# Kernel tuning notes

Measured on AMD Instinct MI355X. Metric: run time of the kernel, lower is better.

Reference implementation:

```python
import jax, jax.numpy as jnp
import numpy as np

NUM_HOPS = 3
NUM_GRAPHS = 2048
N_NODES = 50000
N_EDGES = 2400000
HIDDEN = 128
EMB = 64
N_LAYERS = 3
N_MLP = 2
N_HEADS = 4


def setup_inputs() -> dict:
    key = jax.random.key(0)
    ks = iter(jax.random.split(key, 64))
    nk = lambda: next(ks)
    f = lambda shape: jax.random.normal(nk(), shape, dtype=jnp.float32) * 0.05
    inp = {}
    inp["atom_type"] = jax.random.randint(nk(), (N_NODES,), 0, 100)
    inp["hydrogen_count"] = jax.random.randint(nk(), (N_NODES,), 0, 9)
    inp["degree"] = jax.random.randint(nk(), (N_NODES,), 0, 8)
    inp["hybridization"] = jax.random.randint(nk(), (N_NODES,), 0, 8)
    inp["target"] = jax.random.randint(nk(), (N_EDGES,), 0, NUM_HOPS * N_NODES)
    inp["src"] = jax.random.randint(nk(), (N_EDGES,), 0, NUM_HOPS * N_NODES)
    inp["batch_indices"] = jnp.sort(jax.random.randint(nk(), (N_NODES,), 0, NUM_GRAPHS))
    # learned parameters
    inp["emb_atom"] = f((100, EMB))
    inp["emb_h"] = f((9, EMB))
    inp["emb_deg"] = f((8, EMB))
    inp["emb_hyb"] = f((8, EMB))
    inp["proj_w"] = f((4 * EMB, HIDDEN)); inp["proj_b"] = jnp.zeros((HIDDEN,), jnp.float32)
    IN = HIDDEN * (NUM_HOPS + 1)
    inp["shell_in_w"] = f((N_LAYERS, IN, HIDDEN)); inp["shell_in_b"] = jnp.zeros((N_LAYERS, HIDDEN), jnp.float32)
    inp["shell_mlp_w1"] = f((N_LAYERS, N_MLP, HIDDEN, HIDDEN)); inp["shell_mlp_b1"] = jnp.zeros((N_LAYERS, N_MLP, HIDDEN), jnp.float32)
    inp["shell_mlp_w2"] = f((N_LAYERS, N_MLP, HIDDEN, HIDDEN)); inp["shell_mlp_b2"] = jnp.zeros((N_LAYERS, N_MLP, HIDDEN), jnp.float32)
    inp["shell_skip_w"] = f((N_LAYERS, IN, HIDDEN)); inp["shell_skip_b"] = jnp.zeros((N_LAYERS, HIDDEN), jnp.float32)
    inp["attn_w"] = f((N_HEADS, HIDDEN)); inp["attn_b"] = jnp.zeros((N_HEADS,), jnp.float32)
    inp["temperature"] = jnp.array(1.0, jnp.float32)
    inp["ffn_w1"] = f((HIDDEN, HIDDEN)); inp["ffn_b1"] = jnp.zeros((HIDDEN,), jnp.float32)
    inp["ffn_w2"] = f((HIDDEN, HIDDEN)); inp["ffn_b2"] = jnp.zeros((HIDDEN,), jnp.float32)
    inp["ffn_w3"] = f((HIDDEN, 1)); inp["ffn_b3"] = jnp.zeros((1,), jnp.float32)
    return inp


def _forward(atom_type, hydrogen_count, degree, hybridization, target, src, batch_indices,
             emb_atom, emb_h, emb_deg, emb_hyb, proj_w, proj_b,
             shell_in_w, shell_in_b, shell_mlp_w1, shell_mlp_b1, shell_mlp_w2, shell_mlp_b2,
             shell_skip_w, shell_skip_b, attn_w, attn_b, temperature,
             ffn_w1, ffn_b1, ffn_w2, ffn_b2, ffn_w3, ffn_b3):
    act = jax.nn.silu
    n = atom_type.shape[0]
    # atom embedding: concat of 4 lookups -> projection (dropout off / eval mode)
    emb = jnp.concatenate([emb_atom[atom_type], emb_h[hydrogen_count],
                           emb_deg[degree], emb_hyb[hybridization]], axis=-1)  # [N, 4*EMB]
    x = act(emb @ proj_w + proj_b)  # [N, H]
    for l in range(N_LAYERS):
        # shell convolution: hop aggregation via gather + index_add over expanded [hops*N, H]
        expanded = jnp.tile(x, (NUM_HOPS, 1))                              # [hops*N, H]
        agg = jnp.zeros_like(expanded).at[target].add(expanded[src])
        hops = agg.reshape(NUM_HOPS, n, HIDDEN)                            # split into hop chunks
        feats = jnp.concatenate([x[None], hops], axis=0)                   # [hops+1, N, H]
        feats = jnp.moveaxis(feats, 0, 1).reshape(n, (NUM_HOPS + 1) * HIDDEN)  # cat([x, hop0..], -1)
        h = act(feats @ shell_in_w[l] + shell_in_b[l])
        gskip = feats @ shell_skip_w[l] + shell_skip_b[l]
        for m in range(N_MLP):
            skip = h
            h = act(h @ shell_mlp_w1[l, m] + shell_mlp_b1[l, m])
            h = h @ shell_mlp_w2[l, m] + shell_mlp_b2[l, m]
            h = h + skip
        x = h + gskip
    # multi-head attention pooling with scatter-softmax over graphs
    scores = (x @ attn_w.T + attn_b) / temperature                         # [N, heads]
    smax = jax.ops.segment_max(scores, batch_indices, num_segments=NUM_GRAPHS)
    ex = jnp.exp(scores - smax[batch_indices])
    denom = jax.ops.segment_sum(ex, batch_indices, num_segments=NUM_GRAPHS)
    w = ex / denom[batch_indices]                                          # [N, heads]
    weighted = (x[:, None, :] * w[:, :, None]).reshape(n, N_HEADS * HIDDEN)
    pooled = jax.ops.segment_sum(weighted, batch_indices, num_segments=NUM_GRAPHS)
    pooled = pooled.reshape(NUM_GRAPHS, N_HEADS, HIDDEN).mean(axis=1)      # mean over heads
    # FFN readout
    h = act(pooled @ ffn_w1 + ffn_b1)
    h = act(h @ ffn_w2 + ffn_b2)
    return h @ ffn_w3 + ffn_b3                                             # [G, 1]


def reference(atom_type, hydrogen_count, degree, hybridization, target, src, batch_indices,
              emb_atom, emb_h, emb_deg, emb_hyb, proj_w, proj_b,
              shell_in_w, shell_in_b, shell_mlp_w1, shell_mlp_b1, shell_mlp_w2, shell_mlp_b2,
              shell_skip_w, shell_skip_b, attn_w, attn_b, temperature,
              ffn_w1, ffn_b1, ffn_w2, ffn_b2, ffn_w3, ffn_b3):
    return _forward(atom_type, hydrogen_count, degree, hybridization, target, src, batch_indices,
                    emb_atom, emb_h, emb_deg, emb_hyb, proj_w, proj_b,
                    shell_in_w, shell_in_b, shell_mlp_w1, shell_mlp_b1, shell_mlp_w2, shell_mlp_b2,
                    shell_skip_w, shell_skip_b, attn_w, attn_b, temperature,
                    ffn_w1, ffn_b1, ffn_w2, ffn_b2, ffn_w3, ffn_b3)
```

## Files before the change

### kernel.cpp

```cpp
#include <hip/hip_runtime.h>
#include <math.h>

#define NN      50000
#define NNP     50048
#define NE      2400000
#define NHOPS   3
#define NG      2048
#define H       128
#define EMBD    64
#define NL      3
#define NMLP    2
#define NHEADS  4
#define NROWS   (NHOPS * NN)
#define BINSH   9
#define NBIN    293
#define CAPB    12288
#define ABLK    1024
#define DEPTH   32
#define STG     6144
#define LSTR    136
#define SENT    0xFFFFFFFFu

typedef __bf16 bf16x8 __attribute__((ext_vector_type(8)));
typedef __bf16 bf16x4 __attribute__((ext_vector_type(4)));
typedef float  f32x4  __attribute__((ext_vector_type(4)));

__device__ __forceinline__ float silu_f(float v) { return v / (1.0f + expf(-v)); }

__device__ __forceinline__ f32x4 mm(bf16x8 a, bf16x8 b, f32x4 c) {
    return __builtin_amdgcn_mfma_f32_16x16x32_bf16(a, b, c, 0, 0, 0);
}

__device__ __forceinline__ float blo(unsigned v) { return __builtin_bit_cast(float, v << 16); }
__device__ __forceinline__ float bhi(unsigned v) { return __builtin_bit_cast(float, v & 0xffff0000u); }
__device__ __forceinline__ unsigned pk2(float a, float b) {
    unsigned short ua = __builtin_bit_cast(unsigned short, (__bf16)a);
    unsigned short ub = __builtin_bit_cast(unsigned short, (__bf16)b);
    return (unsigned)ua | ((unsigned)ub << 16);
}

__device__ __forceinline__ void packw_elem(
    const float* __restrict__ W, __bf16* __restrict__ out, int K, long idx)
{
    long per = (long)K * 128;
    long mat = idx / per, e = idx - mat * per;
    int j = (int)(e & 7), n16 = (int)((e >> 3) & 15), q = (int)((e >> 7) & 3),
        mt = (int)((e >> 9) & 7), kt = (int)(e >> 12);
    int k = kt * 32 + q * 8 + j, n = mt * 16 + n16;
    out[idx] = (__bf16)W[mat * per + (long)k * 128 + n];
}

__global__ __launch_bounds__(256) void k_packall(
    const float* __restrict__ projW, __bf16* __restrict__ pproj,
    const float* __restrict__ sInW,  __bf16* __restrict__ pin,
    const float* __restrict__ sSkW,  __bf16* __restrict__ psk,
    const float* __restrict__ mW1,   __bf16* __restrict__ pw1,
    const float* __restrict__ mW2,   __bf16* __restrict__ pw2,
    const float* __restrict__ Ea, const float* __restrict__ Eh,
    const float* __restrict__ Ed, const float* __restrict__ Ey,
    __bf16* __restrict__ embb)
{
    long tid = (long)blockIdx.x * 256 + threadIdx.x;
    if (tid < 32768) { packw_elem(projW, pproj, 256, tid); return; }
    tid -= 32768;
    if (tid < 196608) { packw_elem(sInW, pin, 512, tid); return; }
    tid -= 196608;
    if (tid < 196608) { packw_elem(sSkW, psk, 512, tid); return; }
    tid -= 196608;
    if (tid < 98304) { packw_elem(mW1, pw1, 128, tid); return; }
    tid -= 98304;
    if (tid < 98304) { packw_elem(mW2, pw2, 128, tid); return; }
    tid -= 98304;
    if (tid < 8000) {
        int t = (int)tid;
        float v;
        if (t < 6400) v = Ea[t];
        else if (t < 6976) v = Eh[t - 6400];
        else if (t < 7488) v = Ed[t - 6976];
        else v = Ey[t - 7488];
        embb[t] = (__bf16)v;
    }
}

__global__ __launch_bounds__(256) void k_embed_m(
    const int* __restrict__ atom, const int* __restrict__ hc,
    const int* __restrict__ deg,  const int* __restrict__ hyb,
    const __bf16* __restrict__ emb, const __bf16* __restrict__ pw,
    const float* __restrict__ pb, __bf16* __restrict__ x)
{
    const int lane = threadIdx.x & 63, wid = threadIdx.x >> 6;
    const int q = lane >> 4, l16 = lane & 15;
    const int nb = blockIdx.x * 128 + wid * 32;
    int ia[2][4];
#pragma unroll
    for (int nt = 0; nt < 2; ++nt) {
        int n = nb + nt * 16 + l16;
        if (n >= NN) n = NN - 1;
        ia[nt][0] = atom[n]; ia[nt][1] = hc[n]; ia[nt][2] = deg[n]; ia[nt][3] = hyb[n];
    }
    f32x4 acc[2][8];
#pragma unroll
    for (int nt = 0; nt < 2; ++nt)
#pragma unroll
        for (int mt = 0; mt < 8; ++mt) acc[nt][mt] = (f32x4)(0.f);
    const int tb[4] = {0, 6400, 6976, 7488};
    for (int kt = 0; kt < 8; ++kt) {
        int t = kt >> 1;
        int koff = (kt & 1) * 32 + q * 8;
        bf16x8 bfrag[2];
#pragma unroll
        for (int nt = 0; nt < 2; ++nt)
            bfrag[nt] = *(const bf16x8*)(emb + tb[t] + (long)ia[nt][t] * 64 + koff);
        const __bf16* ap = pw + (long)kt * 4096 + lane * 8;
#pragma unroll
        for (int mt = 0; mt < 8; ++mt) {
            bf16x8 a = *(const bf16x8*)(ap + mt * 512);
            acc[0][mt] = mm(a, bfrag[0], acc[0][mt]);
            acc[1][mt] = mm(a, bfrag[1], acc[1][mt]);
        }
    }
#pragma unroll
    for (int nt = 0; nt < 2; ++nt) {
        long node = nb + nt * 16 + l16;
#pragma unroll
        for (int mt = 0; mt < 8; ++mt) {
            int ch = mt * 16 + q * 4;
            float4 bb = *(const float4*)(pb + ch);
            bf16x4 o;
            o[0] = (__bf16)silu_f(acc[nt][mt][0] + bb.x);
            o[1] = (__bf16)silu_f(acc[nt][mt][1] + bb.y);
            o[2] = (__bf16)silu_f(acc[nt][mt][2] + bb.z);
            o[3] = (__bf16)silu_f(acc[nt][mt][3] + bb.w);
            *(bf16x4*)(x + node * 128 + ch) = o;
        }
    }
}

__global__ __launch_bounds__(256) void k_binA(
    const int* __restrict__ target, const int* __restrict__ src,
    int* __restrict__ gbincur, int* __restrict__ brealc,
    unsigned int* __restrict__ binreg)
{
    __shared__ unsigned int buf[NBIN][DEPTH];
    __shared__ int cnt[NBIN];
    __shared__ int flushed[NBIN];
    const int tid = threadIdx.x;
    for (int i = tid; i < NBIN; i += 256) { cnt[i] = 0; flushed[i] = 0; }
    __syncthreads();
    const int per = (NE + ABLK - 1) / ABLK;
    const int e0 = blockIdx.x * per;
    const int e1 = (e0 + per < NE) ? e0 + per : NE;
    for (int base = e0; base < e1; base += 256) {
        int e = base + tid;
        if (e < e1) {
            int s = src[e];
            if (s >= 2 * NN) s -= 2 * NN; else if (s >= NN) s -= NN;
            int t = target[e];
            int bin = t >> BINSH;
            unsigned val = (unsigned)s | ((unsigned)(t & ((1 << BINSH) - 1)) << 16);
            int slot = atomicAdd(&cnt[bin], 1);
            buf[bin][slot & (DEPTH - 1)] = val;
        }
        __syncthreads();
        for (int b = tid; b < NBIN; b += 256) {
            while (cnt[b] - flushed[b] >= 16) {
                int pos = atomicAdd(&gbincur[b], 16);
                if (pos + 16 <= CAPB) {
                    uint4* d4 = (uint4*)(binreg + (long)b * CAPB + pos);
                    const uint4* s4 = (const uint4*)&buf[b][flushed[b] & (DEPTH - 1)];
                    d4[0] = s4[0]; d4[1] = s4[1]; d4[2] = s4[2]; d4[3] = s4[3];
                }
                flushed[b] += 16;
            }
        }
        __syncthreads();
    }
    for (int b = tid; b < NBIN; b += 256) {
        int lvl = cnt[b] - flushed[b];
        if (cnt[b] > 0) atomicAdd(&brealc[b], cnt[b]);
        if (lvl > 0) {
            int pad = (lvl + 3) & ~3;
            int pos = atomicAdd(&gbincur[b], pad);
            for (int i = 0; i < pad; i += 4) {
                uint4 v;
                v.x = (i + 0 < lvl) ? buf[b][(flushed[b] + i + 0) & (DEPTH - 1)] : SENT;
                v.y = (i + 1 < lvl) ? buf[b][(flushed[b] + i + 1) & (DEPTH - 1)] : SENT;
                v.z = (i + 2 < lvl) ? buf[b][(flushed[b] + i + 2) & (DEPTH - 1)] : SENT;
                v.w = (i + 3 < lvl) ? buf[b][(flushed[b] + i + 3) & (DEPTH - 1)] : SENT;
                if (pos + i + 4 <= CAPB)
                    *(uint4*)(binreg + (long)b * CAPB + pos + i) = v;
            }
        }
    }
}

__global__ __launch_bounds__(512) void k_fill2b(
    const unsigned int* __restrict__ binreg, const int* __restrict__ gbincur,
    const int* __restrict__ brealc, int* __restrict__ csr_start,
    unsigned short* __restrict__ esrc)
{
    __shared__ unsigned int stage[STG];
    __shared__ int pc[512], rcnt[256], scn[256], cur[256];
    __shared__ int nstage;
    const int blk = blockIdx.x;
    const int b = blk >> 1, half = blk & 1;
    const int tid = threadIdx.x;
    int pv = (tid < NBIN) ? brealc[tid] : 0;
    if (pv < 0) pv = 0;
    pc[tid] = pv;
    if (tid == 0) nstage = 0;
    if (tid < 256) rcnt[tid] = 0;
    __syncthreads();
    for (int off = 1; off < 512; off <<= 1) {
        int t = (tid >= off) ? pc[tid - off] : 0;
        __syncthreads();
        pc[tid] += t;
        __syncthreads();
    }
    const int bbase = (b == 0) ? 0 : pc[b - 1];
    const int breal = pc[b] - bbase;
    int total = gbincur[b];
    if (total > CAPB) total = CAPB;
    if (total < 0) total = 0;
    const unsigned int* seg = binreg + (long)b * CAPB;
    for (int i = tid; i < total; i += 512) {
        unsigned pk = seg[i];
        if (pk == SENT) continue;
        int tl = (pk >> 16) & 511;
        if ((tl >> 8) == half) {
            int p = atomicAdd(&nstage, 1);
            if (p < STG) stage[p] = pk;
            atomicAdd(&rcnt[tl & 255], 1);
        }
    }
    __syncthreads();
    int own = nstage; if (own > STG) own = STG;
    const int base0 = bbase + (half ? (breal - own) : 0);
    if (tid < 256) scn[tid] = rcnt[tid];
    __syncthreads();
    for (int off = 1; off < 256; off <<= 1) {
        int t = (tid >= off && tid < 256) ? scn[tid - off] : 0;
        __syncthreads();
        if (tid < 256) scn[tid] += t;
        __syncthreads();
    }
    if (tid < 256) {
        int v = rcnt[tid];
        int rb = base0 + scn[tid] - v;
        cur[tid] = rb;
        int row = b * 512 + half * 256 + tid;
        if (row <= NROWS) csr_start[row] = rb;
    }
    __syncthreads();
    for (int i = tid; i < own; i += 512) {
        unsigned pk = stage[i];
        int pos = atomicAdd(&cur[(pk >> 16) & 255], 1);
        if (pos >= 0 && pos < NE) esrc[pos] = (unsigned short)(pk & 0xffffu);
    }
}

__global__ __launch_bounds__(256) void k_gather(
    const unsigned short* __restrict__ esrc, const int* __restrict__ csr_start,
    const uint4* __restrict__ x8, uint4* __restrict__ agg8)
{
    int row = blockIdx.x * 16 + (threadIdx.x >> 4);
    int lane = threadIdx.x & 63;
    int l4 = lane & 15, qw = lane >> 4;
    int e0 = csr_start[row], e1 = csr_start[row + 1];
    if ((unsigned)e0 > NE || (unsigned)e1 > NE || e1 < e0) { e0 = 0; e1 = 0; }
    int nch = (e1 - e0 + 15) >> 4;
    int n0 = __shfl(nch, 0, 64), n1 = __shfl(nch, 16, 64);
    int n2 = __shfl(nch, 32, 64), n3 = __shfl(nch, 48, 64);
    int nmax = max(max(n0, n1), max(n2, n3));
    float a0 = 0.f, a1 = 0.f, a2 = 0.f, a3 = 0.f, a4 = 0.f, a5 = 0.f, a6 = 0.f, a7 = 0.f;
    const int sb = qw << 4;
    for (int c = 0; c < nmax; ++c) {
        int base = e0 + c * 16;
        int rem = e1 - base;
        int pre = (l4 < rem) ? (int)esrc[base + l4] : 0;
        int m = rem < 16 ? (rem < 0 ? 0 : rem) : 16;
        int j = 0;
        for (; j + 3 < m; j += 4) {
            int sA = __shfl(pre, sb + j, 64);
            int sB = __shfl(pre, sb + j + 1, 64);
            int sC = __shfl(pre, sb + j + 2, 64);
            int sD = __shfl(pre, sb + j + 3, 64);
            uint4 v0 = x8[(long)sA * 16 + l4];
            uint4 v1 = x8[(long)sB * 16 + l4];
            uint4 v2 = x8[(long)sC * 16 + l4];
            uint4 v3 = x8[(long)sD * 16 + l4];
            a0 += blo(v0.x) + blo(v1.x) + blo(v2.x) + blo(v3.x);
            a1 += bhi(v0.x) + bhi(v1.x) + bhi(v2.x) + bhi(v3.x);
            a2 += blo(v0.y) + blo(v1.y) + blo(v2.y) + blo(v3.y);
            a3 += bhi(v0.y) + bhi(v1.y) + bhi(v2.y) + bhi(v3.y);
            a4 += blo(v0.z) + blo(v1.z) + blo(v2.z) + blo(v3.z);
            a5 += bhi(v0.z) + bhi(v1.z) + bhi(v2.z) + bhi(v3.z);
            a6 += blo(v0.w) + blo(v1.w) + blo(v2.w) + blo(v3.w);
            a7 += bhi(v0.w) + bhi(v1.w) + bhi(v2.w) + bhi(v3.w);
        }
        for (; j < m; ++j) {
            int sA = __shfl(pre, sb + j, 64);
            uint4 v0 = x8[(long)sA * 16 + l4];
            a0 += blo(v0.x); a1 += bhi(v0.x); a2 += blo(v0.y); a3 += bhi(v0.y);
            a4 += blo(v0.z); a5 += bhi(v0.z); a6 += blo(v0.w); a7 += bhi(v0.w);
        }
    }
    int hop = row / NN, node = row - hop * NN;
    uint4 o;
    o.x = pk2(a0, a1); o.y = pk2(a2, a3); o.z = pk2(a4, a5); o.w = pk2(a6, a7);
    agg8[((long)hop * NNP + node) * 16 + l4] = o;
}

__global__ __launch_bounds__(128) void k_layer(
    const __bf16* __restrict__ x, const __bf16* __restrict__ agg,
    const __bf16* __restrict__ pwin, const float* __restrict__ bin,
    const __bf16* __restrict__ pwsk, const float* __restrict__ bsk,
    const __bf16* __restrict__ pw1a, const float* __restrict__ b1a,
    const __bf16* __restrict__ pw2a, const float* __restrict__ b2a,
    const __bf16* __restrict__ pw1b, const float* __restrict__ b1b,
    const __bf16* __restrict__ pw2b, const float* __restrict__ b2b,
    __bf16* __restrict__ xout)
{
    __shared__ __bf16 L[16 * LSTR];
    const int lane = threadIdx.x & 63, half = threadIdx.x >> 6;
    const int q = lane >> 4, l16 = lane & 15;
    const int nb = blockIdx.x * 16;
    const int mtoff = half * 4 * 512;
    const int chb = half * 64;
    const int la = lane * 8;
    const long r0 = (long)(nb + l16) * 128;
    const __bf16* planes[4] = {x, agg, agg + (long)NNP * 128, agg + 2L * NNP * 128};

    bf16x8 ring[8];
#pragma unroll
    for (int k = 0; k < 8; ++k)
        ring[k] = *(const bf16x8*)(planes[k >> 2] + (k & 3) * 32 + q * 8 + r0);
    f32x4 aci[4], acs[4];
#pragma unroll
    for (int mt = 0; mt < 4; ++mt) { aci[mt] = (f32x4)(0.f); acs[mt] = (f32x4)(0.f); }
#pragma unroll
    for (int kt = 0; kt < 16; ++kt) {
        bf16x8 b0 = ring[kt & 7];
        if (kt < 8) {
            int k2 = kt + 8;
            ring[kt & 7] = *(const bf16x8*)(planes[k2 >> 2] + (k2 & 3) * 32 + q * 8 + r0);
        }
        const __bf16* aip = pwin + (long)kt * 4096 + mtoff + la;
        const __bf16* asp = pwsk + (long)kt * 4096 + mtoff + la;
#pragma unroll
        for (int mt = 0; mt < 4; ++mt) {
            aci[mt] = mm(*(const bf16x8*)(aip + mt * 512), b0, aci[mt]);
            acs[mt] = mm(*(const bf16x8*)(asp + mt * 512), b0, acs[mt]);
        }
    }
    bf16x4 gk[4];
    bf16x4 hs[4];
#pragma unroll
    for (int mt = 0; mt < 4; ++mt) {
        int ch = chb + mt * 16 + q * 4;
        float4 bi = *(const float4*)(bin + ch);
        float4 bs = *(const float4*)(bsk + ch);
        bf16x4 oh, og;
        oh[0] = (__bf16)silu_f(aci[mt][0] + bi.x);
        oh[1] = (__bf16)silu_f(aci[mt][1] + bi.y);
        oh[2] = (__bf16)silu_f(aci[mt][2] + bi.z);
        oh[3] = (__bf16)silu_f(aci[mt][3] + bi.w);
        og[0] = (__bf16)(acs[mt][0] + bs.x);
        og[1] = (__bf16)(acs[mt][1] + bs.y);
        og[2] = (__bf16)(acs[mt][2] + bs.z);
        og[3] = (__bf16)(acs[mt][3] + bs.w);
        hs[mt] = oh; gk[mt] = og;
        *(bf16x4*)(L + l16 * LSTR + ch) = oh;
    }
    __syncthreads();

    f32x4 acc[4];
    bf16x4 skipreg[4];

#pragma unroll
    for (int mt = 0; mt < 4; ++mt) acc[mt] = (f32x4)(0.f);
#pragma unroll
    for (int kt = 0; kt < 4; ++kt) {
        int koff = kt * 32 + q * 8;
        bf16x8 f0 = *(const bf16x8*)(L + l16 * LSTR + koff);
        const __bf16* ap = pw1a + (long)kt * 4096 + mtoff + la;
#pragma unroll
        for (int mt = 0; mt < 4; ++mt)
            acc[mt] = mm(*(const bf16x8*)(ap + mt * 512), f0, acc[mt]);
    }
    __syncthreads();
#pragma unroll
    for (int mt = 0; mt < 4; ++mt) {
        int ch = chb + mt * 16 + q * 4;
        float4 bb = *(const float4*)(b1a + ch);
        bf16x4 o;
        o[0] = (__bf16)silu_f(acc[mt][0] + bb.x);
        o[1] = (__bf16)silu_f(acc[mt][1] + bb.y);
        o[2] = (__bf16)silu_f(acc[mt][2] + bb.z);
        o[3] = (__bf16)silu_f(acc[mt][3] + bb.w);
        *(bf16x4*)(L + l16 * LSTR + ch) = o;
    }
    __syncthreads();

#pragma unroll
    for (int mt = 0; mt < 4; ++mt) acc[mt] = (f32x4)(0.f);
#pragma unroll
    for (int kt = 0; kt < 4; ++kt) {
        int koff = kt * 32 + q * 8;
        bf16x8 f0 = *(const bf16x8*)(L + l16 * LSTR + koff);
        const __bf16* ap = pw2a + (long)kt * 4096 + mtoff + la;
#pragma unroll
        for (int mt = 0; mt < 4; ++mt)
            acc[mt] = mm(*(const bf16x8*)(ap + mt * 512), f0, acc[mt]);
    }
    __syncthreads();
#pragma unroll
    for (int mt = 0; mt < 4; ++mt) {
        int ch = chb + mt * 16 + q * 4;
        float4 bb = *(const float4*)(b2a + ch);
        bf16x4 sk = hs[mt];
        bf16x4 o;
        o[0] = (__bf16)(acc[mt][0] + bb.x + (float)sk[0]);
        o[1] = (__bf16)(acc[mt][1] + bb.y + (float)sk[1]);
        o[2] = (__bf16)(acc[mt][2] + bb.z + (float)sk[2]);
        o[3] = (__bf16)(acc[mt][3] + bb.w + (float)sk[3]);
        skipreg[mt] = o;
        *(bf16x4*)(L + l16 * LSTR + ch) = o;
    }
    __syncthreads();

#pragma unroll
    for (int mt = 0; mt < 4; ++mt) acc[mt] = (f32x4)(0.f);
#pragma unroll
    for (int kt = 0; kt < 4; ++kt) {
        int koff = kt * 32 + q * 8;
        bf16x8 f0 = *(const bf16x8*)(L + l16 * LSTR + koff);
        const __bf16* ap = pw1b + (long)kt * 4096 + mtoff + la;
#pragma unroll
        for (int mt = 0; mt < 4; ++mt)
            acc[mt] = mm(*(const bf16x8*)(ap + mt * 512), f0, acc[mt]);
    }
    __syncthreads();
#pragma unroll
    for (int mt = 0; mt < 4; ++mt) {
        int ch = chb + mt * 16 + q * 4;
        float4 bb = *(const float4*)(b1b + ch);
        bf16x4 o;
        o[0] = (__bf16)silu_f(acc[mt][0] + bb.x);
        o[1] = (__bf16)silu_f(acc[mt][1] + bb.y);
        o[2] = (__bf16)silu_f(acc[mt][2] + bb.z);
        o[3] = (__bf16)silu_f(acc[mt][3] + bb.w);
        *(bf16x4*)(L + l16 * LSTR + ch) = o;
    }
    __syncthreads();

#pragma unroll
    for (int mt = 0; mt < 4; ++mt) acc[mt] = (f32x4)(0.f);
#pragma unroll
    for (int kt = 0; kt < 4; ++kt) {
        int koff = kt * 32 + q * 8;
        bf16x8 f0 = *(const bf16x8*)(L + l16 * LSTR + koff);
        const __bf16* ap = pw2b + (long)kt * 4096 + mtoff + la;
#pragma unroll
        for (int mt = 0; mt < 4; ++mt)
            acc[mt] = mm(*(const bf16x8*)(ap + mt * 512), f0, acc[mt]);
    }
    long node = nb + l16;
#pragma unroll
    for (int mt = 0; mt < 4; ++mt) {
        int ch = chb + mt * 16 + q * 4;
        float4 bb = *(const float4*)(b2b + ch);
        bf16x4 sk = skipreg[mt];
        bf16x4 g = gk[mt];
        bf16x4 o;
        o[0] = (__bf16)(acc[mt][0] + bb.x + (float)sk[0] + (float)g[0]);
        o[1] = (__bf16)(acc[mt][1] + bb.y + (float)sk[1] + (float)g[1]);
        o[2] = (__bf16)(acc[mt][2] + bb.z + (float)sk[2] + (float)g[2]);
        o[3] = (__bf16)(acc[mt][3] + bb.w + (float)sk[3] + (float)g[3]);
        *(bf16x4*)(xout + node * 128 + ch) = o;
    }
}

__global__ __launch_bounds__(256) void k_scores(
    const __bf16* __restrict__ x, const float* __restrict__ aw,
    const float* __restrict__ ab, const float* __restrict__ temp,
    float* __restrict__ scores)
{
    int wave = threadIdx.x >> 6, lane = threadIdx.x & 63;
    int n = blockIdx.x * 4 + wave;
    if (n >= NN) return;
    float x0 = (float)x[(long)n * H + lane];
    float x1 = (float)x[(long)n * H + 64 + lane];
    float T = temp[0];
#pragma unroll
    for (int hh = 0; hh < NHEADS; ++hh) {
        float p = x0 * aw[hh * H + lane] + x1 * aw[hh * H + 64 + lane];
#pragma unroll
        for (int off = 32; off >= 1; off >>= 1) p += __shfl_xor(p, off, 64);
        if (lane == 0) scores[n * NHEADS + hh] = (p + ab[hh]) / T;
    }
}

__global__ __launch_bounds__(256) void k_offsets(
    const int* __restrict__ batch, int* __restrict__ gstart)
{
    int n = blockIdx.x * 256 + threadIdx.x;
    if (n >= NN) return;
    int b = batch[n];
    int bp = (n == 0) ? -1 : batch[n - 1];
    for (int g = bp + 1; g <= b; ++g) gstart[g] = n;
    if (n == NN - 1) for (int g = b + 1; g <= NG; ++g) gstart[g] = NN;
}

__global__ __launch_bounds__(64) void k_pool(
    const __bf16* __restrict__ x, const float* __restrict__ scores,
    const int* __restrict__ gstart, float* __restrict__ pooled)
{
    int g = blockIdx.x, lane = threadIdx.x;
    int s0 = gstart[g], s1 = gstart[g + 1];
    float m0 = -INFINITY, m1 = -INFINITY, m2 = -INFINITY, m3 = -INFINITY;
    for (int n = s0 + lane; n < s1; n += 64) {
        m0 = fmaxf(m0, scores[n * 4 + 0]); m1 = fmaxf(m1, scores[n * 4 + 1]);
        m2 = fmaxf(m2, scores[n * 4 + 2]); m3 = fmaxf(m3, scores[n * 4 + 3]);
    }
#pragma unroll
    for (int off = 32; off >= 1; off >>= 1) {
        m0 = fmaxf(m0, __shfl_xor(m0, off, 64)); m1 = fmaxf(m1, __shfl_xor(m1, off, 64));
        m2 = fmaxf(m2, __shfl_xor(m2, off, 64)); m3 = fmaxf(m3, __shfl_xor(m3, off, 64));
    }
    float d0 = 0.f, d1 = 0.f, d2 = 0.f, d3 = 0.f;
    for (int n = s0 + lane; n < s1; n += 64) {
        d0 += expf(scores[n * 4 + 0] - m0); d1 += expf(scores[n * 4 + 1] - m1);
        d2 += expf(scores[n * 4 + 2] - m2); d3 += expf(scores[n * 4 + 3] - m3);
    }
#pragma unroll
    for (int off = 32; off >= 1; off >>= 1) {
        d0 += __shfl_xor(d0, off, 64); d1 += __shfl_xor(d1, off, 64);
        d2 += __shfl_xor(d2, off, 64); d3 += __shfl_xor(d3, off, 64);
    }
    float i0 = d0 > 0.f ? 1.f / d0 : 0.f;
    float i1 = d1 > 0.f ? 1.f / d1 : 0.f;
    float i2 = d2 > 0.f ? 1.f / d2 : 0.f;
    float i3 = d3 > 0.f ? 1.f / d3 : 0.f;
    float a0 = 0.f, a1 = 0.f;
    for (int n = s0; n < s1; ++n) {
        float wb = expf(scores[n * 4 + 0] - m0) * i0 + expf(scores[n * 4 + 1] - m1) * i1
                 + expf(scores[n * 4 + 2] - m2) * i2 + expf(scores[n * 4 + 3] - m3) * i3;
        wb *= 0.25f;
        a0 += wb * (float)x[(long)n * H + lane];
        a1 += wb * (float)x[(long)n * H + 64 + lane];
    }
    pooled[g * H + lane] = a0;
    pooled[g * H + 64 + lane] = a1;
}

__global__ __launch_bounds__(128) void k_ffn(
    const float* __restrict__ pooled,
    const float* __restrict__ W1, const float* __restrict__ B1,
    const float* __restrict__ W2, const float* __restrict__ B2,
    const float* __restrict__ W3, const float* __restrict__ B3,
    float* __restrict__ out)
{
    __shared__ float p[H], t1[H], t2[H], red[H];
    int g = blockIdx.x, c = threadIdx.x;
    p[c] = pooled[g * H + c];
    __syncthreads();
    float acc = 0.f;
    for (int k = 0; k < H; ++k) acc += p[k] * W1[k * H + c];
    t1[c] = silu_f(acc + B1[c]);
    __syncthreads();
    acc = 0.f;
    for (int k = 0; k < H; ++k) acc += t1[k] * W2[k * H + c];
    t2[c] = silu_f(acc + B2[c]);
    __syncthreads();
    red[c] = t2[c] * W3[c];
    __syncthreads();
    for (int off = 64; off >= 1; off >>= 1) {
        if (c < off) red[c] += red[c + off];
        __syncthreads();
    }
    if (c == 0) out[g] = red[0] + B3[0];
}

extern "C" void kernel_launch(void* const* d_in, const int* in_sizes, int n_in,
                              void* d_out, int out_size, void* d_ws, size_t ws_size,
                              hipStream_t stream)
{
    const int*   atom   = (const int*)d_in[0];
    const int*   hc     = (const int*)d_in[1];
    const int*   deg    = (const int*)d_in[2];
    const int*   hyb    = (const int*)d_in[3];
    const int*   target = (const int*)d_in[4];
    const int*   src    = (const int*)d_in[5];
    const int*   batch  = (const int*)d_in[6];
    const float* Ea     = (const float*)d_in[7];
    const float* Eh     = (const float*)d_in[8];
    const float* Ed     = (const float*)d_in[9];
    const float* Ey     = (const float*)d_in[10];
    const float* projW  = (const float*)d_in[11];
    const float* projB  = (const float*)d_in[12];
    const float* sInW   = (const float*)d_in[13];
    const float* sInB   = (const float*)d_in[14];
    const float* mW1    = (const float*)d_in[15];
    const float* mB1    = (const float*)d_in[16];
    const float* mW2    = (const float*)d_in[17];
    const float* mB2    = (const float*)d_in[18];
    const float* sSkW   = (const float*)d_in[19];
    const float* sSkB   = (const float*)d_in[20];
    const float* attnW  = (const float*)d_in[21];
    const float* attnB  = (const float*)d_in[22];
    const float* temp   = (const float*)d_in[23];
    const float* fW1    = (const float*)d_in[24];
    const float* fB1    = (const float*)d_in[25];
    const float* fW2    = (const float*)d_in[26];
    const float* fB2    = (const float*)d_in[27];
    const float* fW3    = (const float*)d_in[28];
    const float* fB3    = (const float*)d_in[29];
    float* out = (float*)d_out;

    char* w = (char*)d_ws;
    auto take = [&](size_t bytes) { void* p = (void*)w; w += (bytes + 255) & ~(size_t)255; return p; };
    __bf16* x      = (__bf16*)take(2L * NNP * H);
    __bf16* agg    = (__bf16*)take(2L * 3 * NNP * H);
    __bf16* pproj  = (__bf16*)take(2L * 256 * H);
    __bf16* pin    = (__bf16*)take(2L * 3 * 512 * H);
    __bf16* psk    = (__bf16*)take(2L * 3 * 512 * H);
    __bf16* pw1    = (__bf16*)take(2L * 6 * 128 * H);
    __bf16* pw2    = (__bf16*)take(2L * 6 * 128 * H);
    __bf16* embb   = (__bf16*)take(2L * 8000);
    float*  scores = (float*)take(4L * NN * NHEADS);
    float*  pooled = (float*)take(4L * NG * H);
    int*    gstart = (int*)take(4L * (NG + 1));
    int*    csr_start = (int*)take(4L * (NROWS + 1));
    unsigned int*   binreg = (unsigned int*)take(4L * NBIN * CAPB);
    unsigned short* esrc   = (unsigned short*)take(2L * NE);
    int*    gbincur = (int*)take(4L * 2 * NBIN);
    int*    brealc  = gbincur + NBIN;

    k_packall<<<(630592 + 255) / 256, 256, 0, stream>>>(
        projW, pproj, sInW, pin, sSkW, psk, mW1, pw1, mW2, pw2,
        Ea, Eh, Ed, Ey, embb);

    hipMemsetAsync(gbincur, 0, sizeof(int) * 2 * NBIN, stream);
    k_binA<<<ABLK, 256, 0, stream>>>(target, src, gbincur, brealc, binreg);
    k_fill2b<<<2 * NBIN, 512, 0, stream>>>(binreg, gbincur, brealc, csr_start, esrc);

    k_embed_m<<<NNP / 128, 256, 0, stream>>>(atom, hc, deg, hyb, embb, pproj, projB, x);
    k_offsets<<<(NN + 255) / 256, 256, 0, stream>>>(batch, gstart);

    for (int l = 0; l < NL; ++l) {
        k_gather<<<NROWS / 16, 256, 0, stream>>>(esrc, csr_start,
            (const uint4*)x, (uint4*)agg);
        k_layer<<<NNP / 16, 128, 0, stream>>>(x, agg,
            pin + (long)l * 512 * H, sInB + l * H,
            psk + (long)l * 512 * H, sSkB + l * H,
            pw1 + (long)(l * NMLP + 0) * 128 * H, mB1 + (long)(l * NMLP + 0) * H,
            pw2 + (long)(l * NMLP + 0) * 128 * H, mB2 + (long)(l * NMLP + 0) * H,
            pw1 + (long)(l * NMLP + 1) * 128 * H, mB1 + (long)(l * NMLP + 1) * H,
            pw2 + (long)(l * NMLP + 1) * 128 * H, mB2 + (long)(l * NMLP + 1) * H,
            x);
    }

    k_scores<<<NN / 4, 256, 0, stream>>>(x, attnW, attnB, temp, scores);
    k_pool<<<NG, 64, 0, stream>>>(x, scores, gstart, pooled);
    k_ffn<<<NG, 128, 0, stream>>>(pooled, fW1, fB1, fW2, fB2, fW3, fB3, out);
}
```

Measured before the change: 657.9 us.

## Fuse neighbor gather into layer kernel via shared-memory aggregates and ping-pong x

```diff
diff --git a/kernel.cpp b/kernel.cpp
--- a/kernel.cpp
+++ b/kernel.cpp
@@ -19,6 +19,7 @@
 #define DEPTH   32
 #define STG     6144
 #define LSTR    136
+#define AGSTR   136
 #define SENT    0xFFFFFFFFu
 
 typedef __bf16 bf16x8 __attribute__((ext_vector_type(8)));
@@ -259,60 +260,9 @@
     }
 }
 
-__global__ __launch_bounds__(256) void k_gather(
+__global__ __launch_bounds__(128) void k_layer_g(
     const unsigned short* __restrict__ esrc, const int* __restrict__ csr_start,
-    const uint4* __restrict__ x8, uint4* __restrict__ agg8)
-{
-    int row = blockIdx.x * 16 + (threadIdx.x >> 4);
-    int lane = threadIdx.x & 63;
-    int l4 = lane & 15, qw = lane >> 4;
-    int e0 = csr_start[row], e1 = csr_start[row + 1];
-    if ((unsigned)e0 > NE || (unsigned)e1 > NE || e1 < e0) { e0 = 0; e1 = 0; }
-    int nch = (e1 - e0 + 15) >> 4;
-    int n0 = __shfl(nch, 0, 64), n1 = __shfl(nch, 16, 64);
-    int n2 = __shfl(nch, 32, 64), n3 = __shfl(nch, 48, 64);
-    int nmax = max(max(n0, n1), max(n2, n3));
-    float a0 = 0.f, a1 = 0.f, a2 = 0.f, a3 = 0.f, a4 = 0.f, a5 = 0.f, a6 = 0.f, a7 = 0.f;
-    const int sb = qw << 4;
-    for (int c = 0; c < nmax; ++c) {
-        int base = e0 + c * 16;
-        int rem = e1 - base;
-        int pre = (l4 < rem) ? (int)esrc[base + l4] : 0;
-        int m = rem < 16 ? (rem < 0 ? 0 : rem) : 16;
-        int j = 0;
-        for (; j + 3 < m; j += 4) {
-            int sA = __shfl(pre, sb + j, 64);
-            int sB = __shfl(pre, sb + j + 1, 64);
-            int sC = __shfl(pre, sb + j + 2, 64);
-            int sD = __shfl(pre, sb + j + 3, 64);
-            uint4 v0 = x8[(long)sA * 16 + l4];
-            uint4 v1 = x8[(long)sB * 16 + l4];
-            uint4 v2 = x8[(long)sC * 16 + l4];
-            uint4 v3 = x8[(long)sD * 16 + l4];
-            a0 += blo(v0.x) + blo(v1.x) + blo(v2.x) + blo(v3.x);
-            a1 += bhi(v0.x) + bhi(v1.x) + bhi(v2.x) + bhi(v3.x);
-            a2 += blo(v0.y) + blo(v1.y) + blo(v2.y) + blo(v3.y);
-            a3 += bhi(v0.y) + bhi(v1.y) + bhi(v2.y) + bhi(v3.y);
-            a4 += blo(v0.z) + blo(v1.z) + blo(v2.z) + blo(v3.z);
-            a5 += bhi(v0.z) + bhi(v1.z) + bhi(v2.z) + bhi(v3.z);
-            a6 += blo(v0.w) + blo(v1.w) + blo(v2.w) + blo(v3.w);
-            a7 += bhi(v0.w) + bhi(v1.w) + bhi(v2.w) + bhi(v3.w);
-        }
-        for (; j < m; ++j) {
-            int sA = __shfl(pre, sb + j, 64);
-            uint4 v0 = x8[(long)sA * 16 + l4];
-            a0 += blo(v0.x); a1 += bhi(v0.x); a2 += blo(v0.y); a3 += bhi(v0.y);
-            a4 += blo(v0.z); a5 += bhi(v0.z); a6 += blo(v0.w); a7 += bhi(v0.w);
-        }
-    }
-    int hop = row / NN, node = row - hop * NN;
-    uint4 o;
-    o.x = pk2(a0, a1); o.y = pk2(a2, a3); o.z = pk2(a4, a5); o.w = pk2(a6, a7);
-    agg8[((long)hop * NNP + node) * 16 + l4] = o;
-}
-
-__global__ __launch_bounds__(128) void k_layer(
-    const __bf16* __restrict__ x, const __bf16* __restrict__ agg,
+    const __bf16* __restrict__ x,
     const __bf16* __restrict__ pwin, const float* __restrict__ bin,
     const __bf16* __restrict__ pwsk, const float* __restrict__ bsk,
     const __bf16* __restrict__ pw1a, const float* __restrict__ b1a,
@@ -321,7 +271,7 @@
     const __bf16* __restrict__ pw2b, const float* __restrict__ b2b,
     __bf16* __restrict__ xout)
 {
-    __shared__ __bf16 L[16 * LSTR];
+    __shared__ __bf16 AG[48 * AGSTR];
     const int lane = threadIdx.x & 63, half = threadIdx.x >> 6;
     const int q = lane >> 4, l16 = lane & 15;
     const int nb = blockIdx.x * 16;
@@ -329,21 +279,82 @@
     const int chb = half * 64;
     const int la = lane * 8;
     const long r0 = (long)(nb + l16) * 128;
-    const __bf16* planes[4] = {x, agg, agg + (long)NNP * 128, agg + 2L * NNP * 128};
-
-    bf16x8 ring[8];
-#pragma unroll
-    for (int k = 0; k < 8; ++k)
-        ring[k] = *(const bf16x8*)(planes[k >> 2] + (k & 3) * 32 + q * 8 + r0);
+    const uint4* x8 = (const uint4*)x;
+
+    {
+        const int l4 = lane & 15, qw = lane >> 4;
+        const int sb = qw << 4;
+#pragma unroll
+        for (int p = 0; p < 6; ++p) {
+            int ridx = half * 24 + p * 4 + qw;
+            int hop = ridx >> 4, nloc = ridx & 15;
+            int node = nb + nloc;
+            int e0 = 0, e1 = 0;
+            if (node < NN) {
+                int grow = hop * NN + node;
+                e0 = csr_start[grow]; e1 = csr_start[grow + 1];
+                if ((unsigned)e0 > NE || (unsigned)e1 > NE || e1 < e0) { e0 = 0; e1 = 0; }
+            }
+            int nch = (e1 - e0 + 15) >> 4;
+            int n0 = __shfl(nch, sb - sb + (half ? 32 : 0) + 0, 64);
+            n0 = __shfl(nch, 0, 64);
+            int n1 = __shfl(nch, 16, 64);
+            int n2 = __shfl(nch, 32, 64);
+            int n3 = __shfl(nch, 48, 64);
+            int nmax = max(max(n0, n1), max(n2, n3));
+            float a0 = 0.f, a1 = 0.f, a2 = 0.f, a3 = 0.f, a4 = 0.f, a5 = 0.f, a6 = 0.f, a7 = 0.f;
+            for (int c = 0; c < nmax; ++c) {
+                int base = e0 + c * 16;
+                int rem = e1 - base;
+                int pre = (l4 < rem) ? (int)esrc[base + l4] : 0;
+                int m = rem < 16 ? (rem < 0 ? 0 : rem) : 16;
+                int j = 0;
+                for (; j + 3 < m; j += 4) {
+                    int sA = __shfl(pre, sb + j, 64);
+                    int sB = __shfl(pre, sb + j + 1, 64);
+                    int sC = __shfl(pre, sb + j + 2, 64);
+                    int sD = __shfl(pre, sb + j + 3, 64);
+                    uint4 v0 = x8[(long)sA * 16 + l4];
+                    uint4 v1 = x8[(long)sB * 16 + l4];
+                    uint4 v2 = x8[(long)sC * 16 + l4];
+                    uint4 v3 = x8[(long)sD * 16 + l4];
+                    a0 += blo(v0.x) + blo(v1.x) + blo(v2.x) + blo(v3.x);
+                    a1 += bhi(v0.x) + bhi(v1.x) + bhi(v2.x) + bhi(v3.x);
+                    a2 += blo(v0.y) + blo(v1.y) + blo(v2.y) + blo(v3.y);
+                    a3 += bhi(v0.y) + bhi(v1.y) + bhi(v2.y) + bhi(v3.y);
+                    a4 += blo(v0.z) + blo(v1.z) + blo(v2.z) + blo(v3.z);
+                    a5 += bhi(v0.z) + bhi(v1.z) + bhi(v2.z) + bhi(v3.z);
+                    a6 += blo(v0.w) + blo(v1.w) + blo(v2.w) + blo(v3.w);
+                    a7 += bhi(v0.w) + bhi(v1.w) + bhi(v2.w) + bhi(v3.w);
+                }
+                for (; j < m; ++j) {
+                    int sA = __shfl(pre, sb + j, 64);
+                    uint4 v0 = x8[(long)sA * 16 + l4];
+                    a0 += blo(v0.x); a1 += bhi(v0.x); a2 += blo(v0.y); a3 += bhi(v0.y);
+                    a4 += blo(v0.z); a5 += bhi(v0.z); a6 += blo(v0.w); a7 += bhi(v0.w);
+                }
+            }
+            uint4 o;
+            o.x = pk2(a0, a1); o.y = pk2(a2, a3); o.z = pk2(a4, a5); o.w = pk2(a6, a7);
+            *(uint4*)(AG + ridx * AGSTR + l4 * 8) = o;
+        }
+    }
+    __syncthreads();
+
+    bf16x8 ring[4];
+#pragma unroll
+    for (int k = 0; k < 4; ++k)
+        ring[k] = *(const bf16x8*)(x + k * 32 + q * 8 + r0);
     f32x4 aci[4], acs[4];
 #pragma unroll
     for (int mt = 0; mt < 4; ++mt) { aci[mt] = (f32x4)(0.f); acs[mt] = (f32x4)(0.f); }
 #pragma unroll
     for (int kt = 0; kt < 16; ++kt) {
-        bf16x8 b0 = ring[kt & 7];
-        if (kt < 8) {
-            int k2 = kt + 8;
-            ring[kt & 7] = *(const bf16x8*)(planes[k2 >> 2] + (k2 & 3) * 32 + q * 8 + r0);
+        bf16x8 b0;
+        if (kt < 4) b0 = ring[kt];
+        else {
+            int hop = (kt >> 2) - 1;
+            b0 = *(const bf16x8*)(AG + (hop * 16 + l16) * AGSTR + (kt & 3) * 32 + q * 8);
         }
         const __bf16* aip = pwin + (long)kt * 4096 + mtoff + la;
         const __bf16* asp = pwsk + (long)kt * 4096 + mtoff + la;
@@ -355,6 +366,7 @@
     }
     bf16x4 gk[4];
     bf16x4 hs[4];
+    __syncthreads();
 #pragma unroll
     for (int mt = 0; mt < 4; ++mt) {
         int ch = chb + mt * 16 + q * 4;
@@ -370,19 +382,20 @@
         og[2] = (__bf16)(acs[mt][2] + bs.z);
         og[3] = (__bf16)(acs[mt][3] + bs.w);
         hs[mt] = oh; gk[mt] = og;
-        *(bf16x4*)(L + l16 * LSTR + ch) = oh;
+        *(bf16x4*)(AG + l16 * AGSTR + ch) = oh;
     }
     __syncthreads();
 
     f32x4 acc[4];
     bf16x4 skipreg[4];
+    __bf16* L = AG;
 
 #pragma unroll
     for (int mt = 0; mt < 4; ++mt) acc[mt] = (f32x4)(0.f);
 #pragma unroll
     for (int kt = 0; kt < 4; ++kt) {
         int koff = kt * 32 + q * 8;
-        bf16x8 f0 = *(const bf16x8*)(L + l16 * LSTR + koff);
+        bf16x8 f0 = *(const bf16x8*)(L + l16 * AGSTR + koff);
         const __bf16* ap = pw1a + (long)kt * 4096 + mtoff + la;
 #pragma unroll
         for (int mt = 0; mt < 4; ++mt)
@@ -398,7 +411,7 @@
         o[1] = (__bf16)silu_f(acc[mt][1] + bb.y);
         o[2] = (__bf16)silu_f(acc[mt][2] + bb.z);
         o[3] = (__bf16)silu_f(acc[mt][3] + bb.w);
-        *(bf16x4*)(L + l16 * LSTR + ch) = o;
+        *(bf16x4*)(L + l16 * AGSTR + ch) = o;
     }
     __syncthreads();
 
@@ -407,7 +420,7 @@
 #pragma unroll
     for (int kt = 0; kt < 4; ++kt) {
         int koff = kt * 32 + q * 8;
-        bf16x8 f0 = *(const bf16x8*)(L + l16 * LSTR + koff);
+        bf16x8 f0 = *(const bf16x8*)(L + l16 * AGSTR + koff);
         const __bf16* ap = pw2a + (long)kt * 4096 + mtoff + la;
 #pragma unroll
         for (int mt = 0; mt < 4; ++mt)
@@ -425,7 +438,7 @@
         o[2] = (__bf16)(acc[mt][2] + bb.z + (float)sk[2]);
         o[3] = (__bf16)(acc[mt][3] + bb.w + (float)sk[3]);
         skipreg[mt] = o;
-        *(bf16x4*)(L + l16 * LSTR + ch) = o;
+        *(bf16x4*)(L + l16 * AGSTR + ch) = o;
     }
     __syncthreads();
 
@@ -434,7 +447,7 @@
 #pragma unroll
     for (int kt = 0; kt < 4; ++kt) {
         int koff = kt * 32 + q * 8;
-        bf16x8 f0 = *(const bf16x8*)(L + l16 * LSTR + koff);
+        bf16x8 f0 = *(const bf16x8*)(L + l16 * AGSTR + koff);
         const __bf16* ap = pw1b + (long)kt * 4096 + mtoff + la;
 #pragma unroll
         for (int mt = 0; mt < 4; ++mt)
@@ -450,7 +463,7 @@
         o[1] = (__bf16)silu_f(acc[mt][1] + bb.y);
         o[2] = (__bf16)silu_f(acc[mt][2] + bb.z);
         o[3] = (__bf16)silu_f(acc[mt][3] + bb.w);
-        *(bf16x4*)(L + l16 * LSTR + ch) = o;
+        *(bf16x4*)(L + l16 * AGSTR + ch) = o;
     }
     __syncthreads();
 
@@ -459,7 +472,7 @@
 #pragma unroll
     for (int kt = 0; kt < 4; ++kt) {
         int koff = kt * 32 + q * 8;
-        bf16x8 f0 = *(const bf16x8*)(L + l16 * LSTR + koff);
+        bf16x8 f0 = *(const bf16x8*)(L + l16 * AGSTR + koff);
         const __bf16* ap = pw2b + (long)kt * 4096 + mtoff + la;
 #pragma unroll
         for (int mt = 0; mt < 4; ++mt)
@@ -621,7 +634,7 @@
     char* w = (char*)d_ws;
     auto take = [&](size_t bytes) { void* p = (void*)w; w += (bytes + 255) & ~(size_t)255; return p; };
     __bf16* x      = (__bf16*)take(2L * NNP * H);
-    __bf16* agg    = (__bf16*)take(2L * 3 * NNP * H);
+    __bf16* xnew   = (__bf16*)take(2L * NNP * H);
     __bf16* pproj  = (__bf16*)take(2L * 256 * H);
     __bf16* pin    = (__bf16*)take(2L * 3 * 512 * H);
     __bf16* psk    = (__bf16*)take(2L * 3 * 512 * H);
@@ -648,20 +661,21 @@
     k_embed_m<<<NNP / 128, 256, 0, stream>>>(atom, hc, deg, hyb, embb, pproj, projB, x);
     k_offsets<<<(NN + 255) / 256, 256, 0, stream>>>(batch, gstart);
 
+    __bf16* xa = x;
+    __bf16* xb = xnew;
     for (int l = 0; l < NL; ++l) {
-        k_gather<<<NROWS / 16, 256, 0, stream>>>(esrc, csr_start,
-            (const uint4*)x, (uint4*)agg);
-        k_layer<<<NNP / 16, 128, 0, stream>>>(x, agg,
+        k_layer_g<<<NNP / 16, 128, 0, stream>>>(esrc, csr_start, xa,
             pin + (long)l * 512 * H, sInB + l * H,
             psk + (long)l * 512 * H, sSkB + l * H,
             pw1 + (long)(l * NMLP + 0) * 128 * H, mB1 + (long)(l * NMLP + 0) * H,
             pw2 + (long)(l * NMLP + 0) * 128 * H, mB2 + (long)(l * NMLP + 0) * H,
             pw1 + (long)(l * NMLP + 1) * 128 * H, mB1 + (long)(l * NMLP + 1) * H,
             pw2 + (long)(l * NMLP + 1) * 128 * H, mB2 + (long)(l * NMLP + 1) * H,
-            x);
-    }
-
-    k_scores<<<NN / 4, 256, 0, stream>>>(x, attnW, attnB, temp, scores);
-    k_pool<<<NG, 64, 0, stream>>>(x, scores, gstart, pooled);
+            xb);
+        __bf16* t = xa; xa = xb; xb = t;
+    }
+
+    k_scores<<<NN / 4, 256, 0, stream>>>(xa, attnW, attnB, temp, scores);
+    k_pool<<<NG, 64, 0, stream>>>(xa, scores, gstart, pooled);
     k_ffn<<<NG, 128, 0, stream>>>(pooled, fW1, fB1, fW2, fB2, fW3, fB3, out);
 }
```

Measured after the change: 781.8 us. 1.19x slower.
